# Kernel optimization log

Hardware: AMD Instinct MI355X
Metric: run time of the kernel (lower is better)

The kernel has to match this reference:

```python
import jax, jax.numpy as jnp
import numpy as np

HIDDEN = 2880
NUM_HEADS = 64
NUM_KV_HEADS = 8
HEAD_DIM = 64
ROPE_THETA = 150000.0
WINDOW = 128  # sliding window size (attend to last WINDOW tokens incl. current)
SCALE = HEAD_DIM ** -0.5
Q_SIZE = NUM_HEADS * HEAD_DIM          # 4096
KV_SIZE = NUM_KV_HEADS * HEAD_DIM      # 512


def _rope_neox(x, positions):
    # x: [T, n_heads, HEAD_DIM]; neox-style rotary over the full head dim
    half = HEAD_DIM // 2
    inv_freq = 1.0 / (ROPE_THETA ** (jnp.arange(half, dtype=jnp.float32) / half))
    freqs = positions.astype(jnp.float32)[:, None] * inv_freq[None, :]  # [T, half]
    cos = jnp.cos(freqs)[:, None, :]
    sin = jnp.sin(freqs)[:, None, :]
    x1, x2 = x[..., :half], x[..., half:]
    return jnp.concatenate([x1 * cos - x2 * sin, x2 * cos + x1 * sin], axis=-1)


def setup_inputs() -> dict:
    key = jax.random.key(0)
    k1, k2, k3, k4 = jax.random.split(key, 4)
    T = 2048
    hidden_states = jax.random.normal(k1, (T, HIDDEN), dtype=jnp.float32)
    positions = jnp.arange(T, dtype=jnp.int32)
    w_qkv = jax.random.normal(k2, (HIDDEN, Q_SIZE + 2 * KV_SIZE), dtype=jnp.float32) * (HIDDEN ** -0.5)
    w_o = jax.random.normal(k3, (Q_SIZE, HIDDEN), dtype=jnp.float32) * (Q_SIZE ** -0.5)
    sinks = jax.random.normal(k4, (NUM_HEADS,), dtype=jnp.float32)
    return {"positions": positions, "hidden_states": hidden_states,
            "w_qkv": w_qkv, "w_o": w_o, "sinks": sinks}


def reference(positions, hidden_states, w_qkv, w_o, sinks):
    T = hidden_states.shape[0]
    qkv = hidden_states @ w_qkv  # [T, 5120]
    q = qkv[:, :Q_SIZE].reshape(T, NUM_HEADS, HEAD_DIM)
    k = qkv[:, Q_SIZE:Q_SIZE + KV_SIZE].reshape(T, NUM_KV_HEADS, HEAD_DIM)
    v = qkv[:, Q_SIZE + KV_SIZE:].reshape(T, NUM_KV_HEADS, HEAD_DIM)

    q = _rope_neox(q, positions)
    k = _rope_neox(k, positions)

    # GQA: each group of NUM_HEADS//NUM_KV_HEADS query heads shares one kv head
    rep = NUM_HEADS // NUM_KV_HEADS
    k = jnp.repeat(k, rep, axis=1)  # [T, NUM_HEADS, HEAD_DIM]
    v = jnp.repeat(v, rep, axis=1)

    scores = jnp.einsum('qhd,khd->hqk', q, k) * SCALE  # [H, T, T]
    pos_q = positions[:, None]
    pos_k = positions[None, :]
    mask = (pos_k <= pos_q) & (pos_q - pos_k < WINDOW)  # causal + sliding window
    neg = jnp.finfo(scores.dtype).min
    scores = jnp.where(mask[None, :, :], scores, neg)

    # softmax with per-head learned sink logit included in the denominator
    m = jnp.maximum(scores.max(axis=-1), sinks[:, None])      # [H, T]
    e = jnp.exp(scores - m[..., None])                        # [H, T, T]
    denom = e.sum(axis=-1) + jnp.exp(sinks[:, None] - m)      # [H, T]
    probs = e / denom[..., None]

    attn = jnp.einsum('hqk,khd->qhd', probs, v).reshape(T, Q_SIZE)
    return attn @ w_o  # [T, HIDDEN]
```

## Files before the change

kernel.cpp:

```cpp
#include <hip/hip_runtime.h>
#include <hip/hip_bf16.h>

#define T_SEQ   2048
#define HIDDEN  2880
#define NQ      64
#define NKV     8
#define HD      64
#define QSIZE   4096
#define KVSIZE  512
#define QKV_N   5120
#define WINDOW  128
#define SCALE_F 0.125f
#define ROPE_L2 0.53733241958f

typedef unsigned short u16;
typedef __attribute__((ext_vector_type(8))) short short8;
typedef __attribute__((ext_vector_type(4))) float f32x4;

__device__ __forceinline__ u16 f2bf(float f) {
  __hip_bfloat16 b = __float2bfloat16(f);
  u16 u; __builtin_memcpy(&u, &b, 2); return u;
}

__device__ __forceinline__ void gload16(const u16* g, u16* l) {
  __builtin_amdgcn_global_load_lds(
      (const __attribute__((address_space(1))) void*)g,
      (__attribute__((address_space(3))) void*)l, 16, 0, 0);
}

#define CAST_BLKS 5760
#define TQ_BX 80
#define TQ_BLKS (80 * 45)
#define PREP_BLKS (CAST_BLKS + TQ_BLKS)

__global__ void prep_kernel(const float* __restrict__ hidden,
                            const float* __restrict__ w_qkv,
                            u16* __restrict__ Xb, u16* __restrict__ Wqt) {
  __shared__ float tile[64][65];
  const int b = blockIdx.x, tid = threadIdx.x;
  if (b < CAST_BLKS) {
    size_t i = (size_t)b * 256 + tid;
    float4 v = ((const float4*)hidden)[i];
    ushort4 o;
    o.x = f2bf(v.x); o.y = f2bf(v.y); o.z = f2bf(v.z); o.w = f2bf(v.w);
    ((ushort4*)Xb)[i] = o;
    return;
  }
  const int bb = b - CAST_BLKS;
  const int bx = bb % TQ_BX, by = bb / TQ_BX;
  const int r0 = by * 64, c0 = bx * 64;
  const int tx = tid & 15, ty = tid >> 4;
#pragma unroll
  for (int i = 0; i < 4; ++i) {
    float4 v = *(const float4*)(w_qkv + (size_t)(r0 + ty + 16 * i) * QKV_N + c0 + tx * 4);
    tile[tx * 4 + 0][ty + 16 * i] = v.x;
    tile[tx * 4 + 1][ty + 16 * i] = v.y;
    tile[tx * 4 + 2][ty + 16 * i] = v.z;
    tile[tx * 4 + 3][ty + 16 * i] = v.w;
  }
  __syncthreads();
  const int rr8 = (tid & 7) * 8, cc0 = tid >> 3;
#pragma unroll
  for (int p = 0; p < 2; ++p) {
    int cc = cc0 + 32 * p;
    short8 o;
#pragma unroll
    for (int j = 0; j < 8; ++j) o[j] = (short)f2bf(tile[cc][rr8 + j]);
    *(short8*)(Wqt + (size_t)(c0 + cc) * HIDDEN + r0 + rr8) = o;
  }
}

template <int MODE>
__global__ __launch_bounds__(256)
void gemm_bt_kernel(const u16* __restrict__ A, const u16* __restrict__ B,
                    float* __restrict__ Cout, const int* __restrict__ positions,
                    u16* __restrict__ qb, u16* __restrict__ kb,
                    u16* __restrict__ vb, const float* __restrict__ tin,
                    u16* __restrict__ tout, int Kstride, int NKT,
                    int Bvalid, int Nout, int ldc, int NX, int NYC, int NY,
                    int GEMM_BLKS) {
  __shared__ __align__(16) u16 smem[2 * (64 + 128) * 64];
  const int tid = threadIdx.x;
  const int bb = blockIdx.x;

  if (MODE == 1 && bb >= GEMM_BLKS) {
    float (*tile)[65] = (float (*)[65])smem;
    const int bt = bb - GEMM_BLKS;
    const int bx = bt % 45, by = bt / 45;
    const int r0 = by * 64, c0 = bx * 64;
    const int tx = tid & 15, ty = tid >> 4;
#pragma unroll
    for (int i = 0; i < 4; ++i) {
      float4 v = *(const float4*)(tin + (size_t)(r0 + ty + 16 * i) * HIDDEN + c0 + tx * 4);
      tile[tx * 4 + 0][ty + 16 * i] = v.x;
      tile[tx * 4 + 1][ty + 16 * i] = v.y;
      tile[tx * 4 + 2][ty + 16 * i] = v.z;
      tile[tx * 4 + 3][ty + 16 * i] = v.w;
    }
    __syncthreads();
    const int rr8 = (tid & 7) * 8, cc0 = tid >> 3;
#pragma unroll
    for (int p = 0; p < 2; ++p) {
      int cc = cc0 + 32 * p;
      short8 o;
#pragma unroll
      for (int j = 0; j < 8; ++j) o[j] = (short)f2bf(tile[cc][rr8 + j]);
      *(short8*)(tout + (size_t)(c0 + cc) * QSIZE + r0 + rr8) = o;
    }
    return;
  }

  const int xcd = bb & 7, bi = bb >> 3;
  const int ny = xcd * NYC + (bi % NYC);
  const int mx = bi / NYC;
  if (ny >= NY || mx >= NX) return;
  const int m0 = mx * 64, n0 = ny * 128;

  const int lane = tid & 63, wave = tid >> 6;
  const int quad = lane >> 4, l16 = lane & 15;
  const int wm = wave >> 1, wn = wave & 1;

  const int NB = (64 + 128) * 64;
  u16* As = smem;
  u16* Bs = smem + 64 * 64;

  const u16* Aptr[2]; const u16* Bptr[4]; u16* Alds[2]; u16* Blds[4];
#pragma unroll
  for (int it = 0; it < 2; ++it) {
    int c = it * 256 + tid;
    int r = c >> 3;
    int lcol = ((c & 7) ^ (r & 7)) * 8;
    Aptr[it] = A + (size_t)(m0 + r) * Kstride + lcol;
    Alds[it] = As + c * 8;
  }
#pragma unroll
  for (int it = 0; it < 4; ++it) {
    int c = it * 256 + tid;
    int r = c >> 3;
    int lcol = ((c & 7) ^ (r & 7)) * 8;
    int br = n0 + r; br = br < Bvalid ? br : Bvalid - 1;
    Bptr[it] = B + (size_t)br * Kstride + lcol;
    Blds[it] = Bs + c * 8;
  }

  f32x4 acc[2][4] = {};
  const int sw0 = (quad ^ (l16 & 7)) * 8;

#pragma unroll
  for (int it = 0; it < 2; ++it) gload16(Aptr[it], Alds[it]);
#pragma unroll
  for (int it = 0; it < 4; ++it) gload16(Bptr[it], Blds[it]);
  asm volatile("s_waitcnt vmcnt(0)" ::: "memory");
  __syncthreads();

  int cur = 0;
  for (int t = 0; t < NKT; ++t) {
    if (t + 1 < NKT) {
      const int bo = (cur ^ 1) * NB;
      const int ktn = (t + 1) * 64;
#pragma unroll
      for (int it = 0; it < 2; ++it) gload16(Aptr[it] + ktn, Alds[it] + bo);
#pragma unroll
      for (int it = 0; it < 4; ++it) gload16(Bptr[it] + ktn, Blds[it] + bo);
    }
    const u16* Ac = As + cur * NB;
    const u16* Bc = Bs + cur * NB;
#pragma unroll
    for (int kk = 0; kk < 2; ++kk) {
      const int swo = sw0 ^ (kk * 32);
      short8 af[2], bf[4];
#pragma unroll
      for (int i = 0; i < 2; ++i)
        af[i] = *(const short8*)(Ac + (wm * 32 + i * 16 + l16) * 64 + swo);
#pragma unroll
      for (int j = 0; j < 4; ++j)
        bf[j] = *(const short8*)(Bc + (wn * 64 + j * 16 + l16) * 64 + swo);
#pragma unroll
      for (int i = 0; i < 2; ++i)
#pragma unroll
        for (int j = 0; j < 4; ++j)
          acc[i][j] = __builtin_amdgcn_mfma_f32_16x16x32_bf16(af[i], bf[j], acc[i][j], 0, 0, 0);
    }
    if (t + 1 < NKT) {
      asm volatile("s_waitcnt vmcnt(0)" ::: "memory");
      __syncthreads();
      cur ^= 1;
    }
  }

  if (MODE == 0) {
#pragma unroll
    for (int i = 0; i < 2; ++i) {
      const int row = m0 + wm * 32 + i * 16 + quad * 4;
#pragma unroll
      for (int j = 0; j < 4; ++j) {
        const int col = n0 + wn * 64 + j * 16 + l16;
        if (col < Nout)
#pragma unroll
          for (int r = 0; r < 4; ++r)
            Cout[(size_t)(row + r) * ldc + col] = acc[i][j][r];
      }
    }
  } else {
    const int region = (n0 < QSIZE) ? 0 : (n0 < QSIZE + KVSIZE ? 1 : 2);
    if (region <= 1) {
      float invs[2];
#pragma unroll
      for (int j = 0; j < 2; ++j)
        invs[j] = exp2f(-(float)(j * 16 + l16) * ROPE_L2);
#pragma unroll
      for (int i = 0; i < 2; ++i) {
#pragma unroll
        for (int r = 0; r < 4; ++r) {
          const int row = m0 + wm * 32 + i * 16 + quad * 4 + r;
          const float pos = (float)positions[row];
#pragma unroll
          for (int j = 0; j < 2; ++j) {
            float s, c;
            sincosf(pos * invs[j], &s, &c);
            const float x1 = acc[i][j][r], x2 = acc[i][j + 2][r];
            const float o1 = x1 * c - x2 * s, o2 = x2 * c + x1 * s;
            const int col = n0 + wn * 64 + j * 16 + l16;
            if (region == 0) {
              qb[(size_t)row * QSIZE + col] = f2bf(o1);
              qb[(size_t)row * QSIZE + col + 32] = f2bf(o2);
            } else {
              kb[(size_t)row * KVSIZE + col - QSIZE] = f2bf(o1);
              kb[(size_t)row * KVSIZE + col - QSIZE + 32] = f2bf(o2);
            }
          }
        }
      }
    } else {
#pragma unroll
      for (int i = 0; i < 2; ++i) {
        const int row = m0 + wm * 32 + i * 16 + quad * 4;
#pragma unroll
        for (int j = 0; j < 4; ++j) {
          const int col = n0 + wn * 64 + j * 16 + l16 - (QSIZE + KVSIZE);
          ushort4 pk;
          pk.x = f2bf(acc[i][j][0]);
          pk.y = f2bf(acc[i][j][1]);
          pk.z = f2bf(acc[i][j][2]);
          pk.w = f2bf(acc[i][j][3]);
          *(ushort4*)(vb + (size_t)col * T_SEQ + row) = pk;
        }
      }
    }
  }
}

__global__ __launch_bounds__(256, 2)
void attn_kernel(const u16* __restrict__ qb, const u16* __restrict__ kb,
                 const u16* __restrict__ vb_t, const float* __restrict__ sinks,
                 u16* __restrict__ attnb) {
  __shared__ __align__(16) u16 Ks[160 * 72];
  __shared__ __align__(16) u16 Vt[64 * 164];
  __shared__ __align__(16) u16 Pb[4 * 16 * 164];
  const int qt = blockIdx.x, g = blockIdx.y;
  const int q0 = qt * 32, kstart = q0 - 128;
  const int tid = threadIdx.x;
  const int lane = tid & 63, wave = tid >> 6;
  const int quad = lane >> 4, l16 = lane & 15;

  for (int s = tid; s < 1280; s += 256) {
    int r = s >> 3, c8 = (s & 7) * 8;
    int tg = kstart + r; tg = tg < 0 ? 0 : tg;
    *(short8*)(Ks + r * 72 + c8) =
        *(const short8*)(kb + (size_t)tg * KVSIZE + g * HD + c8);
  }
  {
    const int d = tid >> 2, q4 = tid & 3;
    const u16* vrow = vb_t + (size_t)(g * HD + d) * T_SEQ;
#pragma unroll
    for (int it = 0; it < 5; ++it) {
      int k0 = (q4 * 5 + it) * 8;
      int cs = kstart + k0; cs = cs < 0 ? 0 : cs;
      *(short8*)(Vt + d * 164 + k0) = *(const short8*)(vrow + cs);
    }
  }
  __syncthreads();

  short8 bk[10][2];
#pragma unroll
  for (int jf = 0; jf < 10; ++jf)
#pragma unroll
    for (int kk = 0; kk < 2; ++kk)
      bk[jf][kk] = *(const short8*)(Ks + (jf * 16 + l16) * 72 + kk * 32 + quad * 8);

  const int strip = wave & 1, hb = wave >> 1;
  const int qrow0 = q0 + strip * 16;
  u16* Pw = Pb + wave * 16 * 164;
  for (int hh = 0; hh < 4; ++hh) {
    const int h = g * 8 + hb + hh * 2;
    short8 aq[2];
#pragma unroll
    for (int kk = 0; kk < 2; ++kk)
      aq[kk] = *(const short8*)(qb + (size_t)(qrow0 + l16) * QSIZE + h * HD + kk * 32 + quad * 8);
    f32x4 sc[10];
    __builtin_amdgcn_s_setprio(1);
#pragma unroll
    for (int jf = 0; jf < 10; ++jf) {
      f32x4 c = {0.f, 0.f, 0.f, 0.f};
#pragma unroll
      for (int kk = 0; kk < 2; ++kk)
        c = __builtin_amdgcn_mfma_f32_16x16x32_bf16(aq[kk], bk[jf][kk], c, 0, 0, 0);
      sc[jf] = c;
    }
    __builtin_amdgcn_s_setprio(0);

    const float sink = sinks[h];
    float pinv[4];
#pragma unroll
    for (int r = 0; r < 4; ++r) {
      const int qg = qrow0 + quad * 4 + r;
      float mx = -3.0e38f;
#pragma unroll
      for (int jf = 0; jf < 10; ++jf) {
        int kg = kstart + jf * 16 + l16;
        bool valid = (kg >= 0) && (kg <= qg) && (qg - kg < WINDOW);
        float sv = valid ? sc[jf][r] * SCALE_F : -3.0e38f;
        sc[jf][r] = sv;
        mx = fmaxf(mx, sv);
      }
#pragma unroll
      for (int d = 1; d < 16; d <<= 1) mx = fmaxf(mx, __shfl_xor(mx, d, 64));
      mx = fmaxf(mx, sink);
      float sum = 0.f;
#pragma unroll
      for (int jf = 0; jf < 10; ++jf) {
        float e = __expf(sc[jf][r] - mx);
        sc[jf][r] = e;
        sum += e;
      }
#pragma unroll
      for (int d = 1; d < 16; d <<= 1) sum += __shfl_xor(sum, d, 64);
      sum += __expf(sink - mx);
      pinv[r] = 1.0f / sum;
    }

#pragma unroll
    for (int jf = 0; jf < 10; ++jf)
#pragma unroll
      for (int r = 0; r < 4; ++r)
        Pw[(quad * 4 + r) * 164 + jf * 16 + l16] = f2bf(sc[jf][r] * pinv[r]);

    f32x4 o[4] = {};
    __builtin_amdgcn_s_setprio(1);
#pragma unroll
    for (int kk = 0; kk < 5; ++kk) {
      short8 ap = *(const short8*)(Pw + l16 * 164 + kk * 32 + quad * 8);
#pragma unroll
      for (int jf = 0; jf < 4; ++jf) {
        short8 bv = *(const short8*)(Vt + (jf * 16 + l16) * 164 + kk * 32 + quad * 8);
        o[jf] = __builtin_amdgcn_mfma_f32_16x16x32_bf16(ap, bv, o[jf], 0, 0, 0);
      }
    }
    __builtin_amdgcn_s_setprio(0);
#pragma unroll
    for (int jf = 0; jf < 4; ++jf)
#pragma unroll
      for (int r = 0; r < 4; ++r) {
        int qg = qrow0 + quad * 4 + r;
        attnb[(size_t)qg * QSIZE + h * HD + jf * 16 + l16] = f2bf(o[jf][r]);
      }
  }
}

extern "C" void kernel_launch(void* const* d_in, const int* in_sizes, int n_in,
                              void* d_out, int out_size, void* d_ws, size_t ws_size,
                              hipStream_t stream) {
  (void)in_sizes; (void)n_in; (void)out_size; (void)ws_size;
  const int*   positions = (const int*)d_in[0];
  const float* hidden    = (const float*)d_in[1];
  const float* w_qkv     = (const float*)d_in[2];
  const float* w_o       = (const float*)d_in[3];
  const float* sinks     = (const float*)d_in[4];

  char* p = (char*)d_ws;
  u16* Xb    = (u16*)p; p += (size_t)T_SEQ * HIDDEN * 2;
  u16* Wqt   = (u16*)p; p += (size_t)QKV_N * HIDDEN * 2;
  u16* Wot   = (u16*)p; p += (size_t)HIDDEN * QSIZE * 2;
  u16* qb    = (u16*)p; p += (size_t)T_SEQ * QSIZE * 2;
  u16* kb    = (u16*)p; p += (size_t)T_SEQ * KVSIZE * 2;
  u16* vbt   = (u16*)p; p += (size_t)T_SEQ * KVSIZE * 2;
  u16* attnb = (u16*)p; p += (size_t)T_SEQ * QSIZE * 2;

  prep_kernel<<<PREP_BLKS, 256, 0, stream>>>(hidden, w_qkv, Xb, Wqt);
  gemm_bt_kernel<1><<<32 * 8 * 5 + 45 * 64, 256, 0, stream>>>(
      Xb, Wqt, nullptr, positions, qb, kb, vbt, w_o, Wot,
      HIDDEN, 45, QKV_N, QKV_N, QKV_N, 32, 5, 40, 32 * 8 * 5);
  attn_kernel<<<dim3(T_SEQ / 32, NKV), 256, 0, stream>>>(qb, kb, vbt, sinks, attnb);
  gemm_bt_kernel<0><<<32 * 8 * 3, 256, 0, stream>>>(
      attnb, Wot, (float*)d_out, nullptr, nullptr, nullptr, nullptr,
      nullptr, nullptr, QSIZE, 64, HIDDEN, HIDDEN, HIDDEN, 32, 3, 23, 32 * 8 * 3);
}
```

Measured before the change: 315.4 us.

## Enlarge GEMM tiles to 256-wide with 8-wave blocks and MFMA priority hints

Replaces the 64x128 GEMM tile with 256-thread blocks by a templated 8-wave, 512-thread kernel. It uses 256-column tiles, 256 rows for the QKV projection and 128 rows for the output projection. B fragments are held in registers across four A sub-passes, and s_setprio is raised around the MFMA bursts. The XCD-aware block remapping is dropped, and the fused weight-transpose blocks now each handle two tiles. This aims to raise data reuse per LDS load and cut global traffic. The risk is that the grids shrink to 160 and 192 blocks, fewer than the CU count, and the large LDS footprint allows only one block per CU.

```diff
diff --git a/kernel.cpp b/kernel.cpp
--- a/kernel.cpp
+++ b/kernel.cpp
@@ -70,25 +70,28 @@
   }
 }
 
-template <int MODE>
-__global__ __launch_bounds__(256)
-void gemm_bt_kernel(const u16* __restrict__ A, const u16* __restrict__ B,
-                    float* __restrict__ Cout, const int* __restrict__ positions,
-                    u16* __restrict__ qb, u16* __restrict__ kb,
-                    u16* __restrict__ vb, const float* __restrict__ tin,
-                    u16* __restrict__ tout, int Kstride, int NKT,
-                    int Bvalid, int Nout, int ldc, int NX, int NYC, int NY,
-                    int GEMM_BLKS) {
-  __shared__ __align__(16) u16 smem[2 * (64 + 128) * 64];
+template <int MODE, int MFRAG, int AGRP>
+__global__ __launch_bounds__(512, 2)
+void gemm8_kernel(const u16* __restrict__ A, const u16* __restrict__ B,
+                  float* __restrict__ Cout, const int* __restrict__ positions,
+                  u16* __restrict__ qb, u16* __restrict__ kb,
+                  u16* __restrict__ vb, const float* __restrict__ tin,
+                  u16* __restrict__ tout, int Kstride, int NKT,
+                  int Bvalid, int Nout, int ldc, int NYT, int GEMM_BLKS) {
+  constexpr int BM  = MFRAG * 32;
+  constexpr int BUF = (BM + 256) * 64;
+  constexpr int MQ  = MFRAG / 4;
+  __shared__ __align__(16) u16 smem[2 * BUF];
   const int tid = threadIdx.x;
   const int bb = blockIdx.x;
 
   if (MODE == 1 && bb >= GEMM_BLKS) {
-    float (*tile)[65] = (float (*)[65])smem;
-    const int bt = bb - GEMM_BLKS;
-    const int bx = bt % 45, by = bt / 45;
+    const int half = tid >> 8, t2 = (bb - GEMM_BLKS) * 2 + half;
+    const int tl = tid & 255;
+    float (*tile)[65] = (float (*)[65])(smem + half * (64 * 65 * 2));
+    const int bx = t2 % 45, by = t2 / 45;
     const int r0 = by * 64, c0 = bx * 64;
-    const int tx = tid & 15, ty = tid >> 4;
+    const int tx = tl & 15, ty = tl >> 4;
 #pragma unroll
     for (int i = 0; i < 4; ++i) {
       float4 v = *(const float4*)(tin + (size_t)(r0 + ty + 16 * i) * HIDDEN + c0 + tx * 4);
@@ -98,7 +101,7 @@
       tile[tx * 4 + 3][ty + 16 * i] = v.w;
     }
     __syncthreads();
-    const int rr8 = (tid & 7) * 8, cc0 = tid >> 3;
+    const int rr8 = (tl & 7) * 8, cc0 = tl >> 3;
 #pragma unroll
     for (int p = 0; p < 2; ++p) {
       int cc = cc0 + 32 * p;
@@ -110,88 +113,86 @@
     return;
   }
 
-  const int xcd = bb & 7, bi = bb >> 3;
-  const int ny = xcd * NYC + (bi % NYC);
-  const int mx = bi / NYC;
-  if (ny >= NY || mx >= NX) return;
-  const int m0 = mx * 64, n0 = ny * 128;
+  const int mx = bb / NYT, ny = bb % NYT;
+  const int m0 = mx * BM, n0 = ny * 256;
 
   const int lane = tid & 63, wave = tid >> 6;
   const int quad = lane >> 4, l16 = lane & 15;
-  const int wm = wave >> 1, wn = wave & 1;
-
-  const int NB = (64 + 128) * 64;
-  u16* As = smem;
-  u16* Bs = smem + 64 * 64;
-
-  const u16* Aptr[2]; const u16* Bptr[4]; u16* Alds[2]; u16* Blds[4];
-#pragma unroll
-  for (int it = 0; it < 2; ++it) {
-    int c = it * 256 + tid;
+  const int wm = wave >> 2, wn = wave & 3;
+
+  const u16* gpa[AGRP]; const u16* gpb[4]; int aoff[AGRP], boff[4];
+#pragma unroll
+  for (int g = 0; g < AGRP; ++g) {
+    int c = g * 512 + tid;
     int r = c >> 3;
     int lcol = ((c & 7) ^ (r & 7)) * 8;
-    Aptr[it] = A + (size_t)(m0 + r) * Kstride + lcol;
-    Alds[it] = As + c * 8;
-  }
-#pragma unroll
-  for (int it = 0; it < 4; ++it) {
-    int c = it * 256 + tid;
+    gpa[g] = A + (size_t)(m0 + r) * Kstride + lcol;
+    aoff[g] = c * 8;
+  }
+#pragma unroll
+  for (int g = 0; g < 4; ++g) {
+    int c = g * 512 + tid;
     int r = c >> 3;
     int lcol = ((c & 7) ^ (r & 7)) * 8;
     int br = n0 + r; br = br < Bvalid ? br : Bvalid - 1;
-    Bptr[it] = B + (size_t)br * Kstride + lcol;
-    Blds[it] = Bs + c * 8;
-  }
-
-  f32x4 acc[2][4] = {};
+    gpb[g] = B + (size_t)br * Kstride + lcol;
+    boff[g] = BM * 64 + c * 8;
+  }
+
+  auto STAGE = [&](int t, u16* base) {
+    const int kt = t * 64;
+#pragma unroll
+    for (int g = 0; g < AGRP; ++g) gload16(gpa[g] + kt, base + aoff[g]);
+#pragma unroll
+    for (int g = 0; g < 4; ++g) gload16(gpb[g] + kt, base + boff[g]);
+  };
+
+  f32x4 acc[MFRAG][4] = {};
   const int sw0 = (quad ^ (l16 & 7)) * 8;
 
-#pragma unroll
-  for (int it = 0; it < 2; ++it) gload16(Aptr[it], Alds[it]);
-#pragma unroll
-  for (int it = 0; it < 4; ++it) gload16(Bptr[it], Blds[it]);
-  asm volatile("s_waitcnt vmcnt(0)" ::: "memory");
+  STAGE(0, smem);
   __syncthreads();
 
-  int cur = 0;
   for (int t = 0; t < NKT; ++t) {
-    if (t + 1 < NKT) {
-      const int bo = (cur ^ 1) * NB;
-      const int ktn = (t + 1) * 64;
-#pragma unroll
-      for (int it = 0; it < 2; ++it) gload16(Aptr[it] + ktn, Alds[it] + bo);
-#pragma unroll
-      for (int it = 0; it < 4; ++it) gload16(Bptr[it] + ktn, Blds[it] + bo);
-    }
-    const u16* Ac = As + cur * NB;
-    const u16* Bc = Bs + cur * NB;
+    u16* bufr = smem + (t & 1) * BUF;
+    if (t + 1 < NKT) STAGE(t + 1, smem + ((t + 1) & 1) * BUF);
+
+    short8 bfr[4][2];
 #pragma unroll
     for (int kk = 0; kk < 2; ++kk) {
       const int swo = sw0 ^ (kk * 32);
-      short8 af[2], bf[4];
-#pragma unroll
-      for (int i = 0; i < 2; ++i)
-        af[i] = *(const short8*)(Ac + (wm * 32 + i * 16 + l16) * 64 + swo);
 #pragma unroll
       for (int j = 0; j < 4; ++j)
-        bf[j] = *(const short8*)(Bc + (wn * 64 + j * 16 + l16) * 64 + swo);
-#pragma unroll
-      for (int i = 0; i < 2; ++i)
-#pragma unroll
-        for (int j = 0; j < 4; ++j)
-          acc[i][j] = __builtin_amdgcn_mfma_f32_16x16x32_bf16(af[i], bf[j], acc[i][j], 0, 0, 0);
-    }
-    if (t + 1 < NKT) {
-      asm volatile("s_waitcnt vmcnt(0)" ::: "memory");
-      __syncthreads();
-      cur ^= 1;
-    }
+        bfr[j][kk] = *(const short8*)(bufr + BM * 64 + (wn * 64 + j * 16 + l16) * 64 + swo);
+    }
+#pragma unroll
+    for (int q = 0; q < 4; ++q) {
+      short8 af[MQ][2];
+#pragma unroll
+      for (int kk = 0; kk < 2; ++kk) {
+        const int swo = sw0 ^ (kk * 32);
+#pragma unroll
+        for (int im = 0; im < MQ; ++im)
+          af[im][kk] = *(const short8*)(bufr + (wm * MFRAG * 16 + (q * MQ + im) * 16 + l16) * 64 + swo);
+      }
+      __builtin_amdgcn_s_setprio(1);
+#pragma unroll
+      for (int kk = 0; kk < 2; ++kk)
+#pragma unroll
+        for (int im = 0; im < MQ; ++im)
+#pragma unroll
+          for (int j = 0; j < 4; ++j)
+            acc[q * MQ + im][j] =
+                __builtin_amdgcn_mfma_f32_16x16x32_bf16(af[im][kk], bfr[j][kk], acc[q * MQ + im][j], 0, 0, 0);
+      __builtin_amdgcn_s_setprio(0);
+    }
+    if (t + 1 < NKT) __syncthreads();
   }
 
   if (MODE == 0) {
 #pragma unroll
-    for (int i = 0; i < 2; ++i) {
-      const int row = m0 + wm * 32 + i * 16 + quad * 4;
+    for (int i = 0; i < MFRAG; ++i) {
+      const int row = m0 + wm * MFRAG * 16 + i * 16 + quad * 4;
 #pragma unroll
       for (int j = 0; j < 4; ++j) {
         const int col = n0 + wn * 64 + j * 16 + l16;
@@ -209,10 +210,10 @@
       for (int j = 0; j < 2; ++j)
         invs[j] = exp2f(-(float)(j * 16 + l16) * ROPE_L2);
 #pragma unroll
-      for (int i = 0; i < 2; ++i) {
+      for (int i = 0; i < MFRAG; ++i) {
 #pragma unroll
         for (int r = 0; r < 4; ++r) {
-          const int row = m0 + wm * 32 + i * 16 + quad * 4 + r;
+          const int row = m0 + wm * MFRAG * 16 + i * 16 + quad * 4 + r;
           const float pos = (float)positions[row];
 #pragma unroll
           for (int j = 0; j < 2; ++j) {
@@ -233,8 +234,8 @@
       }
     } else {
 #pragma unroll
-      for (int i = 0; i < 2; ++i) {
-        const int row = m0 + wm * 32 + i * 16 + quad * 4;
+      for (int i = 0; i < MFRAG; ++i) {
+        const int row = m0 + wm * MFRAG * 16 + i * 16 + quad * 4;
 #pragma unroll
         for (int j = 0; j < 4; ++j) {
           const int col = n0 + wn * 64 + j * 16 + l16 - (QSIZE + KVSIZE);
@@ -387,11 +388,11 @@
   u16* attnb = (u16*)p; p += (size_t)T_SEQ * QSIZE * 2;
 
   prep_kernel<<<PREP_BLKS, 256, 0, stream>>>(hidden, w_qkv, Xb, Wqt);
-  gemm_bt_kernel<1><<<32 * 8 * 5 + 45 * 64, 256, 0, stream>>>(
+  gemm8_kernel<1, 8, 4><<<160 + 1440, 512, 0, stream>>>(
       Xb, Wqt, nullptr, positions, qb, kb, vbt, w_o, Wot,
-      HIDDEN, 45, QKV_N, QKV_N, QKV_N, 32, 5, 40, 32 * 8 * 5);
+      HIDDEN, 45, QKV_N, QKV_N, QKV_N, 20, 160);
   attn_kernel<<<dim3(T_SEQ / 32, NKV), 256, 0, stream>>>(qb, kb, vbt, sinks, attnb);
-  gemm_bt_kernel<0><<<32 * 8 * 3, 256, 0, stream>>>(
+  gemm8_kernel<0, 4, 2><<<16 * 12, 512, 0, stream>>>(
       attnb, Wot, (float*)d_out, nullptr, nullptr, nullptr, nullptr,
-      nullptr, nullptr, QSIZE, 64, HIDDEN, HIDDEN, HIDDEN, 32, 3, 23, 32 * 8 * 3);
-}
+      nullptr, nullptr, QSIZE, 64, HIDDEN, HIDDEN, HIDDEN, 12, 16 * 12);
+}
```

Measured after the change: 1.080 ms. 242% more time.

## Widen GEMM tile to 64x256 with single-buffered LDS and three blocks per CU

Applied to the files above, without the earlier changes.

The GEMM kernel now computes a 64x256 tile per block, with each wave owning a 64-column slice, instead of a 64x128 tile. The double-buffered LDS pipeline is replaced by a single buffer sized for the larger tile, and launch bounds request three blocks per CU. Grid sizes for the QKV and output GEMMs are adjusted to match. The goal is more data reuse per block and higher occupancy to hide latency in place of explicit prefetch. In exchange, loads are no longer overlapped with MFMA inside a block, and register pressure rises from the larger accumulator array.

```diff
diff --git a/kernel.cpp b/kernel.cpp
--- a/kernel.cpp
+++ b/kernel.cpp
@@ -71,7 +71,7 @@
 }
 
 template <int MODE>
-__global__ __launch_bounds__(256)
+__global__ __launch_bounds__(256, 3)
 void gemm_bt_kernel(const u16* __restrict__ A, const u16* __restrict__ B,
                     float* __restrict__ Cout, const int* __restrict__ positions,
                     u16* __restrict__ qb, u16* __restrict__ kb,
@@ -79,7 +79,7 @@
                     u16* __restrict__ tout, int Kstride, int NKT,
                     int Bvalid, int Nout, int ldc, int NX, int NYC, int NY,
                     int GEMM_BLKS) {
-  __shared__ __align__(16) u16 smem[2 * (64 + 128) * 64];
+  __shared__ __align__(16) u16 smem[(64 + 256) * 64];
   const int tid = threadIdx.x;
   const int bb = blockIdx.x;
 
@@ -114,17 +114,15 @@
   const int ny = xcd * NYC + (bi % NYC);
   const int mx = bi / NYC;
   if (ny >= NY || mx >= NX) return;
-  const int m0 = mx * 64, n0 = ny * 128;
+  const int m0 = mx * 64, n0 = ny * 256;
 
   const int lane = tid & 63, wave = tid >> 6;
   const int quad = lane >> 4, l16 = lane & 15;
-  const int wm = wave >> 1, wn = wave & 1;
-
-  const int NB = (64 + 128) * 64;
+
   u16* As = smem;
   u16* Bs = smem + 64 * 64;
 
-  const u16* Aptr[2]; const u16* Bptr[4]; u16* Alds[2]; u16* Blds[4];
+  const u16* Aptr[2]; const u16* Bptr[8]; u16* Alds[2]; u16* Blds[8];
 #pragma unroll
   for (int it = 0; it < 2; ++it) {
     int c = it * 256 + tid;
@@ -134,7 +132,7 @@
     Alds[it] = As + c * 8;
   }
 #pragma unroll
-  for (int it = 0; it < 4; ++it) {
+  for (int it = 0; it < 8; ++it) {
     int c = it * 256 + tid;
     int r = c >> 3;
     int lcol = ((c & 7) ^ (r & 7)) * 8;
@@ -143,58 +141,42 @@
     Blds[it] = Bs + c * 8;
   }
 
-  f32x4 acc[2][4] = {};
+  f32x4 acc[4][4] = {};
   const int sw0 = (quad ^ (l16 & 7)) * 8;
 
-#pragma unroll
-  for (int it = 0; it < 2; ++it) gload16(Aptr[it], Alds[it]);
-#pragma unroll
-  for (int it = 0; it < 4; ++it) gload16(Bptr[it], Blds[it]);
-  asm volatile("s_waitcnt vmcnt(0)" ::: "memory");
-  __syncthreads();
-
-  int cur = 0;
-  for (int t = 0; t < NKT; ++t) {
-    if (t + 1 < NKT) {
-      const int bo = (cur ^ 1) * NB;
-      const int ktn = (t + 1) * 64;
-#pragma unroll
-      for (int it = 0; it < 2; ++it) gload16(Aptr[it] + ktn, Alds[it] + bo);
-#pragma unroll
-      for (int it = 0; it < 4; ++it) gload16(Bptr[it] + ktn, Blds[it] + bo);
-    }
-    const u16* Ac = As + cur * NB;
-    const u16* Bc = Bs + cur * NB;
+  for (int t = 0, kt = 0; t < NKT; ++t, kt += 64) {
+#pragma unroll
+    for (int it = 0; it < 2; ++it) gload16(Aptr[it] + kt, Alds[it]);
+#pragma unroll
+    for (int it = 0; it < 8; ++it) gload16(Bptr[it] + kt, Blds[it]);
+    asm volatile("s_waitcnt vmcnt(0)" ::: "memory");
+    __syncthreads();
 #pragma unroll
     for (int kk = 0; kk < 2; ++kk) {
       const int swo = sw0 ^ (kk * 32);
-      short8 af[2], bf[4];
-#pragma unroll
-      for (int i = 0; i < 2; ++i)
-        af[i] = *(const short8*)(Ac + (wm * 32 + i * 16 + l16) * 64 + swo);
+      short8 af[4], bf[4];
+#pragma unroll
+      for (int i = 0; i < 4; ++i)
+        af[i] = *(const short8*)(As + (i * 16 + l16) * 64 + swo);
 #pragma unroll
       for (int j = 0; j < 4; ++j)
-        bf[j] = *(const short8*)(Bc + (wn * 64 + j * 16 + l16) * 64 + swo);
-#pragma unroll
-      for (int i = 0; i < 2; ++i)
+        bf[j] = *(const short8*)(Bs + (wave * 64 + j * 16 + l16) * 64 + swo);
+#pragma unroll
+      for (int i = 0; i < 4; ++i)
 #pragma unroll
         for (int j = 0; j < 4; ++j)
           acc[i][j] = __builtin_amdgcn_mfma_f32_16x16x32_bf16(af[i], bf[j], acc[i][j], 0, 0, 0);
     }
-    if (t + 1 < NKT) {
-      asm volatile("s_waitcnt vmcnt(0)" ::: "memory");
-      __syncthreads();
-      cur ^= 1;
-    }
+    if (t + 1 < NKT) __syncthreads();
   }
 
   if (MODE == 0) {
 #pragma unroll
-    for (int i = 0; i < 2; ++i) {
-      const int row = m0 + wm * 32 + i * 16 + quad * 4;
+    for (int i = 0; i < 4; ++i) {
+      const int row = m0 + i * 16 + quad * 4;
 #pragma unroll
       for (int j = 0; j < 4; ++j) {
-        const int col = n0 + wn * 64 + j * 16 + l16;
+        const int col = n0 + wave * 64 + j * 16 + l16;
         if (col < Nout)
 #pragma unroll
           for (int r = 0; r < 4; ++r)
@@ -209,10 +191,10 @@
       for (int j = 0; j < 2; ++j)
         invs[j] = exp2f(-(float)(j * 16 + l16) * ROPE_L2);
 #pragma unroll
-      for (int i = 0; i < 2; ++i) {
+      for (int i = 0; i < 4; ++i) {
 #pragma unroll
         for (int r = 0; r < 4; ++r) {
-          const int row = m0 + wm * 32 + i * 16 + quad * 4 + r;
+          const int row = m0 + i * 16 + quad * 4 + r;
           const float pos = (float)positions[row];
 #pragma unroll
           for (int j = 0; j < 2; ++j) {
@@ -220,7 +202,7 @@
             sincosf(pos * invs[j], &s, &c);
             const float x1 = acc[i][j][r], x2 = acc[i][j + 2][r];
             const float o1 = x1 * c - x2 * s, o2 = x2 * c + x1 * s;
-            const int col = n0 + wn * 64 + j * 16 + l16;
+            const int col = n0 + wave * 64 + j * 16 + l16;
             if (region == 0) {
               qb[(size_t)row * QSIZE + col] = f2bf(o1);
               qb[(size_t)row * QSIZE + col + 32] = f2bf(o2);
@@ -233,11 +215,11 @@
       }
     } else {
 #pragma unroll
-      for (int i = 0; i < 2; ++i) {
-        const int row = m0 + wm * 32 + i * 16 + quad * 4;
+      for (int i = 0; i < 4; ++i) {
+        const int row = m0 + i * 16 + quad * 4;
 #pragma unroll
         for (int j = 0; j < 4; ++j) {
-          const int col = n0 + wn * 64 + j * 16 + l16 - (QSIZE + KVSIZE);
+          const int col = n0 + wave * 64 + j * 16 + l16 - (QSIZE + KVSIZE);
           ushort4 pk;
           pk.x = f2bf(acc[i][j][0]);
           pk.y = f2bf(acc[i][j][1]);
@@ -387,11 +369,11 @@
   u16* attnb = (u16*)p; p += (size_t)T_SEQ * QSIZE * 2;
 
   prep_kernel<<<PREP_BLKS, 256, 0, stream>>>(hidden, w_qkv, Xb, Wqt);
-  gemm_bt_kernel<1><<<32 * 8 * 5 + 45 * 64, 256, 0, stream>>>(
+  gemm_bt_kernel<1><<<32 * 8 * 3 + 45 * 64, 256, 0, stream>>>(
       Xb, Wqt, nullptr, positions, qb, kb, vbt, w_o, Wot,
-      HIDDEN, 45, QKV_N, QKV_N, QKV_N, 32, 5, 40, 32 * 8 * 5);
+      HIDDEN, 45, QKV_N, QKV_N, QKV_N, 32, 3, 20, 32 * 8 * 3);
   attn_kernel<<<dim3(T_SEQ / 32, NKV), 256, 0, stream>>>(qb, kb, vbt, sinks, attnb);
-  gemm_bt_kernel<0><<<32 * 8 * 3, 256, 0, stream>>>(
+  gemm_bt_kernel<0><<<32 * 8 * 2, 256, 0, stream>>>(
       attnb, Wot, (float*)d_out, nullptr, nullptr, nullptr, nullptr,
-      nullptr, nullptr, QSIZE, 64, HIDDEN, HIDDEN, HIDDEN, 32, 3, 23, 32 * 8 * 3);
-}
+      nullptr, nullptr, QSIZE, 64, HIDDEN, HIDDEN, HIDDEN, 32, 2, 12, 32 * 8 * 2);
+}
```

Measured after the change: 334.1 us. +5.9%, slower.
